# Performance work log

Measured on AMD Instinct MI355X. Metric: run time of the kernel, lower is better.

Reference implementation:

```python
import jax, jax.numpy as jnp
import numpy as np

B, S, H, D = 4, 1024, 20, 64
DM = H * D          # 1280 model dim
DF = 4 * DM         # 5120 ffn dim
EPS = 1e-5          # haiku LayerNorm default


def setup_inputs() -> dict:
    key = jax.random.key(0)
    ks = jax.random.split(key, 12)
    sc = 1.0 / np.sqrt(DM)
    return {
        "x": jax.random.normal(ks[0], (B, S, DM), jnp.float32),
        "ln1_scale": jnp.ones((DM,), jnp.float32),
        "ln1_offset": jnp.zeros((DM,), jnp.float32),
        "wq": jax.random.normal(ks[1], (DM, DM), jnp.float32) * sc,
        "bq": jnp.zeros((DM,), jnp.float32),
        "wk": jax.random.normal(ks[2], (DM, DM), jnp.float32) * sc,
        "bk": jnp.zeros((DM,), jnp.float32),
        "wv": jax.random.normal(ks[3], (DM, DM), jnp.float32) * sc,
        "bv": jnp.zeros((DM,), jnp.float32),
        "wo": jax.random.normal(ks[4], (DM, DM), jnp.float32) * sc,
        "bo": jnp.zeros((DM,), jnp.float32),
        "ln2_scale": jnp.ones((DM,), jnp.float32),
        "ln2_offset": jnp.zeros((DM,), jnp.float32),
        "fc1_w": jax.random.normal(ks[5], (DM, DF), jnp.float32) * sc,
        "fc1_b": jnp.zeros((DF,), jnp.float32),
        "fc2_w": jax.random.normal(ks[6], (DF, DM), jnp.float32) * (1.0 / np.sqrt(DF)),
        "fc2_b": jnp.zeros((DM,), jnp.float32),
    }


def _layer_norm(x, scale, offset):
    m = jnp.mean(x, axis=-1, keepdims=True)
    v = jnp.mean(jnp.square(x - m), axis=-1, keepdims=True)
    return (x - m) * jax.lax.rsqrt(v + EPS) * scale + offset


def reference(x, ln1_scale, ln1_offset, wq, bq, wk, bk, wv, bv, wo, bo,
              ln2_scale, ln2_offset, fc1_w, fc1_b, fc2_w, fc2_b):
    b, s, dm = x.shape
    # --- self-attention sub-block ---
    res = x
    h = _layer_norm(x, ln1_scale, ln1_offset)
    q = (h @ wq + bq).reshape(b, s, H, D)
    k = (h @ wk + bk).reshape(b, s, H, D)
    v = (h @ wv + bv).reshape(b, s, H, D)
    logits = jnp.einsum('bthd,bThd->bhtT', q, k) / jnp.sqrt(jnp.asarray(D, x.dtype))
    weights = jax.nn.softmax(logits, axis=-1)
    attn = jnp.einsum('bhtT,bThd->bthd', weights, v).reshape(b, s, dm)
    x = res + (attn @ wo + bo)
    # --- MLP sub-block ---
    res = x
    h = _layer_norm(x, ln2_scale, ln2_offset)
    h = jax.nn.gelu(h @ fc1_w + fc1_b, approximate=False)
    x = res + (h @ fc2_w + fc2_b)
    return x
```

## Files before the change

### kernel.cpp

```cpp
#include <hip/hip_runtime.h>
#include <hip/hip_bf16.h>

typedef __hip_bfloat16 bf16;
typedef __attribute__((ext_vector_type(8))) short short8;
typedef __attribute__((ext_vector_type(4))) float f32x4;
typedef __attribute__((ext_vector_type(4))) unsigned short u16x4;

#define DMODEL 1280
#define DFFN   5120
#define BATCH  4
#define SEQ    1024
#define NHEAD  20
#define HDIM   64
#define NROWS  (BATCH * SEQ)

#define GLDS(g, l) __builtin_amdgcn_global_load_lds(                            \
    (const __attribute__((address_space(1))) void*)(g),                         \
    (__attribute__((address_space(3))) void*)(l), 16, 0, 0)

static __device__ __forceinline__ short8 ds_read128(const bf16* p) {
    short8 r;
    asm volatile("ds_read_b128 %0, %1"
        : "=v"(r)
        : "v"((const __attribute__((address_space(3))) bf16*)p));
    return r;
}

__global__ __launch_bounds__(256) void prep_all(
    const float* __restrict__ wq, const float* __restrict__ wk,
    const float* __restrict__ wv, const float* __restrict__ wo,
    const float* __restrict__ fc1w, const float* __restrict__ fc2w,
    const float* __restrict__ bq, const float* __restrict__ bk,
    const float* __restrict__ bv,
    bf16* __restrict__ wqkvt, bf16* __restrict__ wot,
    bf16* __restrict__ fc1t, bf16* __restrict__ fc2t,
    float* __restrict__ bqkv)
{
    const int bid = blockIdx.x;
    if (bid == 19200) {
        for (int i = threadIdx.x; i < DMODEL; i += 256) {
            bqkv[i]              = bq[i];
            bqkv[DMODEL + i]     = bk[i];
            bqkv[2 * DMODEL + i] = bv[i];
        }
        return;
    }
    const float* in;
    bf16* out;
    int K, N, n0, k0;
    if (bid < 6400) {
        const int mat = bid / 1600, rem = bid % 1600;
        K = DMODEL; N = DMODEL;
        n0 = (rem % 40) * 32; k0 = (rem / 40) * 32;
        switch (mat) {
            case 0:  in = wq; out = wqkvt; break;
            case 1:  in = wk; out = wqkvt + (size_t)DMODEL * DMODEL; break;
            case 2:  in = wv; out = wqkvt + (size_t)2 * DMODEL * DMODEL; break;
            default: in = wo; out = wot; break;
        }
    } else if (bid < 12800) {
        const int rem = bid - 6400;
        K = DMODEL; N = DFFN; in = fc1w; out = fc1t;
        n0 = (rem % 160) * 32; k0 = (rem / 160) * 32;
    } else {
        const int rem = bid - 12800;
        K = DFFN; N = DMODEL; in = fc2w; out = fc2t;
        n0 = (rem % 40) * 32; k0 = (rem / 40) * 32;
    }
    __shared__ float tile[32][33];
    const int tx = threadIdx.x & 31;
    const int ty = threadIdx.x >> 5;
    for (int i = 0; i < 32; i += 8)
        tile[ty + i][tx] = in[(size_t)(k0 + ty + i) * N + (n0 + tx)];
    __syncthreads();
    for (int i = 0; i < 32; i += 8)
        out[(size_t)(n0 + ty + i) * K + (k0 + tx)] = __float2bfloat16(tile[tx][ty + i]);
}

__global__ __launch_bounds__(256) void ln_bf16(
    const float* __restrict__ x, const float* __restrict__ sc,
    const float* __restrict__ of, bf16* __restrict__ out)
{
    const int row = blockIdx.x;
    const float* xr = x + (size_t)row * DMODEL;
    float v[5];
    float s = 0.f, s2 = 0.f;
    for (int i = 0; i < 5; ++i) {
        v[i] = xr[threadIdx.x + i * 256];
        s += v[i];
        s2 += v[i] * v[i];
    }
    for (int off = 1; off < 64; off <<= 1) {
        s  += __shfl_xor(s, off);
        s2 += __shfl_xor(s2, off);
    }
    __shared__ float red[2][4];
    const int wid = threadIdx.x >> 6;
    if ((threadIdx.x & 63) == 0) { red[0][wid] = s; red[1][wid] = s2; }
    __syncthreads();
    s  = red[0][0] + red[0][1] + red[0][2] + red[0][3];
    s2 = red[1][0] + red[1][1] + red[1][2] + red[1][3];
    const float mean = s * (1.0f / DMODEL);
    const float var  = s2 * (1.0f / DMODEL) - mean * mean;
    const float rstd = rsqrtf(var + 1e-5f);
    for (int i = 0; i < 5; ++i) {
        const int c = threadIdx.x + i * 256;
        const float y = (v[i] - mean) * rstd * sc[c] + of[c];
        out[(size_t)row * DMODEL + c] = __float2bfloat16(y);
    }
}

__global__ __launch_bounds__(256) void reduce2_ln(
    const float* __restrict__ P, const float* __restrict__ bias,
    const float* __restrict__ res, float* __restrict__ x1,
    const float* __restrict__ sc, const float* __restrict__ of,
    bf16* __restrict__ h2)
{
    const int row = blockIdx.x;
    const size_t base = (size_t)row * DMODEL;
    const int MN = NROWS * DMODEL;
    float v[5];
    float s = 0.f, s2 = 0.f;
    for (int i = 0; i < 5; ++i) {
        const int c = threadIdx.x + i * 256;
        const float val = P[base + c] + P[MN + base + c] + bias[c] + res[base + c];
        v[i] = val;
        x1[base + c] = val;
        s += val;
        s2 += val * val;
    }
    for (int off = 1; off < 64; off <<= 1) {
        s  += __shfl_xor(s, off);
        s2 += __shfl_xor(s2, off);
    }
    __shared__ float red[2][4];
    const int wid = threadIdx.x >> 6;
    if ((threadIdx.x & 63) == 0) { red[0][wid] = s; red[1][wid] = s2; }
    __syncthreads();
    s  = red[0][0] + red[0][1] + red[0][2] + red[0][3];
    s2 = red[1][0] + red[1][1] + red[1][2] + red[1][3];
    const float mean = s * (1.0f / DMODEL);
    const float var  = s2 * (1.0f / DMODEL) - mean * mean;
    const float rstd = rsqrtf(var + 1e-5f);
    for (int i = 0; i < 5; ++i) {
        const int c = threadIdx.x + i * 256;
        const float y = (v[i] - mean) * rstd * sc[c] + of[c];
        h2[base + c] = __float2bfloat16(y);
    }
}

template <int EPI>
__global__ __launch_bounds__(512, 4) void gemm_big(
    const bf16* __restrict__ A, const bf16* __restrict__ Bt,
    const float* __restrict__ bias,
    bf16* __restrict__ Cb, float* __restrict__ Cf,
    int M, int N, int K, int klen)
{
    __shared__ bf16 As[2][128][32];
    __shared__ bf16 Bs[2][256][32];
    const int m0 = blockIdx.x * 128;
    const int n0 = blockIdx.y * 256;
    const int z  = blockIdx.z;
    const int kbeg = z * klen;

    const int tid  = threadIdx.x;
    const int lane = tid & 63;
    const int wid  = tid >> 6;
    const int wm   = (wid >> 2) * 64;
    const int wn   = (wid & 3) * 64;
    const int l15  = lane & 15;
    const int lq   = lane >> 4;

    f32x4 acc[4][4];
    #pragma unroll
    for (int i = 0; i < 4; ++i)
        #pragma unroll
        for (int j = 0; j < 4; ++j)
            acc[i][j] = (f32x4){0.f, 0.f, 0.f, 0.f};

    const int cph  = lane & 3;
    const int lrow = wid * 16 + (lane >> 2);
    const int cgl8 = (cph ^ ((lrow >> 1) & 3)) * 8;
    const int lcol = cph * 8;

    const bf16* aT = A  + (size_t)(m0 + lrow) * K + kbeg + cgl8;
    const bf16* bT = Bt + (size_t)(n0 + lrow) * K + kbeg + cgl8;
    const size_t rstep = (size_t)128 * K;

    GLDS(aT,         &As[0][lrow][lcol]);
    GLDS(bT,         &Bs[0][lrow][lcol]);
    GLDS(bT + rstep, &Bs[0][lrow + 128][lcol]);

    const int ca = (lq ^ ((l15 >> 1) & 3)) * 8;
    const int nIter = klen / 32;
    int buf = 0;
    for (int it = 0; it < nIter; ++it) {
        asm volatile("s_waitcnt vmcnt(0)" ::: "memory");
        __builtin_amdgcn_s_barrier();

        if (it + 1 < nIter) {
            const int k1 = (it + 1) * 32;
            GLDS(aT + k1,         &As[buf ^ 1][lrow][lcol]);
            GLDS(bT + k1,         &Bs[buf ^ 1][lrow][lcol]);
            GLDS(bT + k1 + rstep, &Bs[buf ^ 1][lrow + 128][lcol]);
        }

        short8 af[4], bfr[4];
        #pragma unroll
        for (int nt = 0; nt < 4; ++nt)
            bfr[nt] = ds_read128(&Bs[buf][wn + nt * 16 + l15][ca]);
        #pragma unroll
        for (int mt = 0; mt < 4; ++mt)
            af[mt] = ds_read128(&As[buf][wm + mt * 16 + l15][ca]);

        __builtin_amdgcn_s_setprio(1);
        asm volatile("s_waitcnt lgkmcnt(3)" ::: "memory");
        __builtin_amdgcn_sched_barrier(0);
        #pragma unroll
        for (int nt = 0; nt < 4; ++nt)
            acc[0][nt] = __builtin_amdgcn_mfma_f32_16x16x32_bf16(
                af[0], bfr[nt], acc[0][nt], 0, 0, 0);
        asm volatile("s_waitcnt lgkmcnt(2)" ::: "memory");
        __builtin_amdgcn_sched_barrier(0);
        #pragma unroll
        for (int nt = 0; nt < 4; ++nt)
            acc[1][nt] = __builtin_amdgcn_mfma_f32_16x16x32_bf16(
                af[1], bfr[nt], acc[1][nt], 0, 0, 0);
        asm volatile("s_waitcnt lgkmcnt(1)" ::: "memory");
        __builtin_amdgcn_sched_barrier(0);
        #pragma unroll
        for (int nt = 0; nt < 4; ++nt)
            acc[2][nt] = __builtin_amdgcn_mfma_f32_16x16x32_bf16(
                af[2], bfr[nt], acc[2][nt], 0, 0, 0);
        asm volatile("s_waitcnt lgkmcnt(0)" ::: "memory");
        __builtin_amdgcn_sched_barrier(0);
        #pragma unroll
        for (int nt = 0; nt < 4; ++nt)
            acc[3][nt] = __builtin_amdgcn_mfma_f32_16x16x32_bf16(
                af[3], bfr[nt], acc[3][nt], 0, 0, 0);
        __builtin_amdgcn_s_setprio(0);

        buf ^= 1;
    }

    float* Pf = Cf + (size_t)z * M * N;
    #pragma unroll
    for (int mt = 0; mt < 4; ++mt)
        #pragma unroll
        for (int nt = 0; nt < 4; ++nt)
            #pragma unroll
            for (int r = 0; r < 4; ++r) {
                const int row = m0 + wm + mt * 16 + lq * 4 + r;
                const int col = n0 + wn + nt * 16 + l15;
                if (EPI == 0) {
                    const float v = acc[mt][nt][r] + bias[col];
                    Cb[(size_t)row * N + col] = __float2bfloat16(v);
                } else if (EPI == 2) {
                    const float v = acc[mt][nt][r] + bias[col];
                    const float g = 0.5f * v * (1.0f + erff(v * 0.70710678118654752f));
                    Cb[(size_t)row * N + col] = __float2bfloat16(g);
                } else {
                    Pf[(size_t)row * N + col] = acc[mt][nt][r];
                }
            }
}

__global__ __launch_bounds__(256) void reduce2(
    const float* __restrict__ P, const float* __restrict__ bias,
    const float* __restrict__ res, float* __restrict__ out, int MN, int N)
{
    const int i = (blockIdx.x * 256 + threadIdx.x) * 4;
    if (i >= MN) return;
    const float4 p0 = *(const float4*)(P + i);
    const float4 p1 = *(const float4*)(P + MN + i);
    const float4 r  = *(const float4*)(res + i);
    const float4 b  = *(const float4*)(bias + (i % N));
    float4 o;
    o.x = p0.x + p1.x + r.x + b.x;
    o.y = p0.y + p1.y + r.y + b.y;
    o.z = p0.z + p1.z + r.z + b.z;
    o.w = p0.w + p1.w + r.w + b.w;
    *(float4*)(out + i) = o;
}

__global__ __launch_bounds__(256) void flash_attn(
    const bf16* __restrict__ qb, const bf16* __restrict__ kb,
    const bf16* __restrict__ vb, bf16* __restrict__ ob, int ldq)
{
    __shared__ bf16 Ks[2][64][64];
    __shared__ bf16 Vt[64][64];
    __shared__ bf16 Ps[4][16][64];

    const int bh = blockIdx.y;
    const int b  = bh / NHEAD;
    const int hh = bh % NHEAD;
    const int q0 = blockIdx.x * 64;
    const int tid  = threadIdx.x;
    const int lane = tid & 63;
    const int wid  = tid >> 6;
    const int l15  = lane & 15;
    const int lq   = lane >> 4;
    const int key  = l15 & 7;

    short8 qf[2];
    {
        const bf16* qp = qb + (size_t)(b * SEQ + q0 + wid * 16 + l15) * ldq
                         + hh * HDIM + lq * 8;
        for (int kk = 0; kk < 2; ++kk) {
            union { short8 v; bf16 h[8]; } u;
            u.v = *(const short8*)(qp + kk * 32);
            for (int j = 0; j < 8; ++j)
                u.h[j] = __float2bfloat16(__bfloat162float(u.h[j]) * 0.125f);
            qf[kk] = u.v;
        }
    }

    f32x4 o[4];
    for (int dt = 0; dt < 4; ++dt) o[dt] = (f32x4){0.f, 0.f, 0.f, 0.f};
    float lsum = 0.f;

    const int krow  = wid * 8 + (lane >> 3);
    const int kcgl8 = ((lane & 7) ^ (krow & 7)) * 8;
    const int kcph8 = (lane & 7) * 8;
    const int vd0  = (tid & 15) * 4;
    const int vkv0 = (tid >> 4) * 4;

    const bf16* kBase = kb + (size_t)(b * SEQ + krow) * ldq + hh * HDIM + kcgl8;
    const bf16* vBase = vb + (size_t)(b * SEQ + vkv0) * ldq + hh * HDIM + vd0;

    GLDS(kBase,                    &Ks[0][krow][kcph8]);
    GLDS(kBase + (size_t)32 * ldq, &Ks[0][krow + 32][kcph8]);
    u16x4 vr[4];
    for (int j = 0; j < 4; ++j)
        vr[j] = *(const u16x4*)(vBase + (size_t)j * ldq);

    const int nIter = SEQ / 64;
    for (int it = 0; it < nIter; ++it) {
        const int buf = it & 1;
        __syncthreads();
        for (int i = 0; i < 4; ++i) {
            u16x4 w = { vr[0][i], vr[1][i], vr[2][i], vr[3][i] };
            const int p = ((vkv0 >> 3) ^ ((vd0 + i) & 7)) * 8 + (vkv0 & 7);
            *(u16x4*)(&Vt[vd0 + i][p]) = w;
        }
        __syncthreads();

        if (it + 1 < nIter) {
            const size_t off = (size_t)(it + 1) * 64 * ldq;
            GLDS(kBase + off,                    &Ks[buf ^ 1][krow][kcph8]);
            GLDS(kBase + off + (size_t)32 * ldq, &Ks[buf ^ 1][krow + 32][kcph8]);
            for (int j = 0; j < 4; ++j)
                vr[j] = *(const u16x4*)(vBase + off + (size_t)j * ldq);
        }

        for (int mt = 0; mt < 4; ++mt) {
            const bf16* kp = &Ks[buf][mt * 16 + l15][0];
            const short8 kf0 = *(const short8*)(kp + ((0 + lq) ^ key) * 8);
            const short8 kf1 = *(const short8*)(kp + ((4 + lq) ^ key) * 8);
            f32x4 a = (f32x4){0.f, 0.f, 0.f, 0.f};
            a = __builtin_amdgcn_mfma_f32_16x16x32_bf16(kf0, qf[0], a, 0, 0, 0);
            a = __builtin_amdgcn_mfma_f32_16x16x32_bf16(kf1, qf[1], a, 0, 0, 0);
            union { u16x4 v; bf16 h[4]; } pk;
            for (int r = 0; r < 4; ++r) {
                const float p = __expf(a[r]);
                lsum += p;
                pk.h[r] = __float2bfloat16(p);
            }
            const int pc = ((mt * 2 + (lq >> 1)) ^ key) * 8 + (lq & 1) * 4;
            *(u16x4*)(&Ps[wid][l15][pc]) = pk.v;
        }

        for (int kk = 0; kk < 2; ++kk) {
            const short8 pf = *(const short8*)(
                &Ps[wid][l15][((lq + 4 * kk) ^ key) * 8]);
            for (int dt = 0; dt < 4; ++dt) {
                const short8 vf = *(const short8*)(
                    &Vt[dt * 16 + l15][((lq + 4 * kk) ^ key) * 8]);
                o[dt] = __builtin_amdgcn_mfma_f32_16x16x32_bf16(
                    vf, pf, o[dt], 0, 0, 0);
            }
        }
    }

    lsum += __shfl_xor(lsum, 16);
    lsum += __shfl_xor(lsum, 32);
    const float inv_l = 1.0f / lsum;

    const size_t qrow = (size_t)(b * SEQ + q0 + wid * 16 + l15);
    for (int dt = 0; dt < 4; ++dt) {
        union { u16x4 v; bf16 h[4]; } w;
        for (int r = 0; r < 4; ++r)
            w.h[r] = __float2bfloat16(o[dt][r] * inv_l);
        *(u16x4*)(ob + qrow * DMODEL + hh * HDIM + dt * 16 + lq * 4) = w.v;
    }
}

extern "C" void kernel_launch(void* const* d_in, const int* in_sizes, int n_in,
                              void* d_out, int out_size, void* d_ws, size_t ws_size,
                              hipStream_t stream)
{
    (void)in_sizes; (void)n_in; (void)out_size; (void)ws_size;
    const float* x    = (const float*)d_in[0];
    const float* ln1s = (const float*)d_in[1];
    const float* ln1o = (const float*)d_in[2];
    const float* wq   = (const float*)d_in[3];
    const float* bq   = (const float*)d_in[4];
    const float* wk   = (const float*)d_in[5];
    const float* bk   = (const float*)d_in[6];
    const float* wv   = (const float*)d_in[7];
    const float* bv   = (const float*)d_in[8];
    const float* wo   = (const float*)d_in[9];
    const float* bo   = (const float*)d_in[10];
    const float* ln2s = (const float*)d_in[11];
    const float* ln2o = (const float*)d_in[12];
    const float* fc1w = (const float*)d_in[13];
    const float* fc1b = (const float*)d_in[14];
    const float* fc2w = (const float*)d_in[15];
    const float* fc2b = (const float*)d_in[16];
    float* out = (float*)d_out;

    char* wp = (char*)d_ws;
    auto alloc = [&](size_t n) { char* p = wp; wp += (n + 255) & ~(size_t)255; return p; };
    bf16*  wqkvt = (bf16*)alloc((size_t)3 * DMODEL * DMODEL * 2);
    bf16*  wot   = (bf16*)alloc((size_t)DMODEL * DMODEL * 2);
    bf16*  fc1t  = (bf16*)alloc((size_t)DFFN * DMODEL * 2);
    bf16*  fc2t  = (bf16*)alloc((size_t)DMODEL * DFFN * 2);
    float* bqkv  = (float*)alloc((size_t)3 * DMODEL * 4);
    char*  regA  = alloc((size_t)NROWS * DMODEL * 2
                       + (size_t)NROWS * 3 * DMODEL * 2
                       + (size_t)NROWS * DMODEL * 2);
    bf16*  h     = (bf16*)regA;
    bf16*  qkv   = (bf16*)(regA + (size_t)NROWS * DMODEL * 2);
    bf16*  attn  = (bf16*)(regA + (size_t)NROWS * 4 * DMODEL * 2);
    float* part  = (float*)regA;
    bf16*  h2    = (bf16*)alloc((size_t)NROWS * DMODEL * 2);
    bf16*  g     = (bf16*)alloc((size_t)NROWS * DFFN * 2);
    float* x1    = out;

    prep_all<<<19201, 256, 0, stream>>>(
        wq, wk, wv, wo, fc1w, fc2w, bq, bk, bv,
        wqkvt, wot, fc1t, fc2t, bqkv);

    ln_bf16<<<NROWS, 256, 0, stream>>>(x, ln1s, ln1o, h);

    gemm_big<0><<<dim3(NROWS / 128, 3 * DMODEL / 256, 1), 512, 0, stream>>>(
        h, wqkvt, bqkv, qkv, nullptr, NROWS, 3 * DMODEL, DMODEL, DMODEL);

    flash_attn<<<dim3(SEQ / 64, BATCH * NHEAD), 256, 0, stream>>>(
        qkv, qkv + DMODEL, qkv + 2 * DMODEL, attn, 3 * DMODEL);

    gemm_big<3><<<dim3(NROWS / 128, DMODEL / 256, 2), 512, 0, stream>>>(
        attn, wot, nullptr, nullptr, part, NROWS, DMODEL, DMODEL, DMODEL / 2);
    reduce2_ln<<<NROWS, 256, 0, stream>>>(part, bo, x, x1, ln2s, ln2o, h2);

    gemm_big<2><<<dim3(NROWS / 128, DFFN / 256, 1), 512, 0, stream>>>(
        h2, fc1t, fc1b, g, nullptr, NROWS, DFFN, DMODEL, DMODEL);

    gemm_big<3><<<dim3(NROWS / 128, DMODEL / 256, 2), 512, 0, stream>>>(
        g, fc2t, nullptr, nullptr, part, NROWS, DMODEL, DFFN, DFFN / 2);
    reduce2<<<(NROWS * DMODEL / 4 + 255) / 256, 256, 0, stream>>>(
        part, fc2b, x1, out, NROWS * DMODEL, DMODEL);
}
```

Measured before the change: 466.4 us.

## Enlarge GEMM tiles to 256x256x64 with interleaved staging and LDS swizzle

Replaces the 128x256x32 GEMM with a 256x256 tile and K-step 64 kernel. It uses 128 KB of dynamic LDS, double-buffered stages prefetched two steps ahead, and a ping-pong schedule that interleaves A/B stage loads between MFMA quadrants under barriers. The aim is to cut global traffic per FLOP and LDS read overhead per MFMA. The cost is fewer blocks: the smaller GEMMs launch under one block per CU and occupancy drops, and register pressure rises from 32 accumulator tiles.

```diff
diff --git a/kernel.cpp b/kernel.cpp
--- a/kernel.cpp
+++ b/kernel.cpp
@@ -150,15 +150,18 @@
 }
 
 template <int EPI>
-__global__ __launch_bounds__(512, 4) void gemm_big(
+__global__ __launch_bounds__(512, 2) void gemm8p(
     const bf16* __restrict__ A, const bf16* __restrict__ Bt,
     const float* __restrict__ bias,
     bf16* __restrict__ Cb, float* __restrict__ Cf,
     int M, int N, int K, int klen)
 {
-    __shared__ bf16 As[2][128][32];
-    __shared__ bf16 Bs[2][256][32];
-    const int m0 = blockIdx.x * 128;
+    extern __shared__ char smem[];
+    constexpr int SLOT = 256 * 64;
+    bf16* As0 = (bf16*)smem;
+    bf16* Bs0 = As0 + 2 * SLOT;
+
+    const int m0 = blockIdx.x * 256;
     const int n0 = blockIdx.y * 256;
     const int z  = blockIdx.z;
     const int kbeg = z * klen;
@@ -166,86 +169,150 @@
     const int tid  = threadIdx.x;
     const int lane = tid & 63;
     const int wid  = tid >> 6;
-    const int wm   = (wid >> 2) * 64;
+    const int wm   = (wid >> 2) * 128;
     const int wn   = (wid & 3) * 64;
     const int l15  = lane & 15;
     const int lq   = lane >> 4;
 
-    f32x4 acc[4][4];
+    f32x4 acc[8][4];
     #pragma unroll
-    for (int i = 0; i < 4; ++i)
+    for (int i = 0; i < 8; ++i)
         #pragma unroll
         for (int j = 0; j < 4; ++j)
             acc[i][j] = (f32x4){0.f, 0.f, 0.f, 0.f};
 
-    const int cph  = lane & 3;
-    const int lrow = wid * 16 + (lane >> 2);
-    const int cgl8 = (cph ^ ((lrow >> 1) & 3)) * 8;
-    const int lcol = cph * 8;
-
-    const bf16* aT = A  + (size_t)(m0 + lrow) * K + kbeg + cgl8;
-    const bf16* bT = Bt + (size_t)(n0 + lrow) * K + kbeg + cgl8;
-    const size_t rstep = (size_t)128 * K;
-
-    GLDS(aT,         &As[0][lrow][lcol]);
-    GLDS(bT,         &Bs[0][lrow][lcol]);
-    GLDS(bT + rstep, &Bs[0][lrow + 128][lcol]);
-
-    const int ca = (lq ^ ((l15 >> 1) & 3)) * 8;
-    const int nIter = klen / 32;
-    int buf = 0;
-    for (int it = 0; it < nIter; ++it) {
-        asm volatile("s_waitcnt vmcnt(0)" ::: "memory");
+    const int srow = wid * 8 + (lane >> 3);
+    const int scl  = (lane & 7) ^ ((wid & 1) << 2) ^ (lane >> 4);
+    const bf16* aT = A  + (size_t)(m0 + srow) * K + kbeg + scl * 8;
+    const bf16* bT = Bt + (size_t)(n0 + srow) * K + kbeg + scl * 8;
+    const size_t rs64 = (size_t)64 * K;
+    const int dwave = (wid * 8) * 64;
+
+    auto STAGE_A = [&](int tt) {
+        const bf16* s = aT + (size_t)tt * 64;
+        bf16* d = As0 + (tt & 1) * SLOT + dwave;
+        GLDS(s,            d);
+        GLDS(s +     rs64, d +  64 * 64);
+        GLDS(s + 2 * rs64, d + 128 * 64);
+        GLDS(s + 3 * rs64, d + 192 * 64);
+    };
+    auto STAGE_B = [&](int tt) {
+        const bf16* s = bT + (size_t)tt * 64;
+        bf16* d = Bs0 + (tt & 1) * SLOT + dwave;
+        GLDS(s,            d);
+        GLDS(s +     rs64, d +  64 * 64);
+        GLDS(s + 2 * rs64, d + 128 * 64);
+        GLDS(s + 3 * rs64, d + 192 * 64);
+    };
+
+    const int rkey = (l15 >> 1) & 7;
+    const int pc0  = ((0 + lq) ^ rkey) * 8;
+    const int pc1  = ((4 + lq) ^ rkey) * 8;
+
+    STAGE_A(0); STAGE_B(0);
+    STAGE_A(1); STAGE_B(1);
+    asm volatile("s_waitcnt vmcnt(8)" ::: "memory");
+    __builtin_amdgcn_s_barrier();
+
+    const int T = klen / 64;
+    for (int t = 0; t < T; ++t) {
+        const int sl = t & 1;
+        bf16* Ac = As0 + sl * SLOT;
+        bf16* Bc = Bs0 + sl * SLOT;
+
+        short8 af[4][2], b0[2][2], b1[2][2];
+
+        #pragma unroll
+        for (int mt = 0; mt < 4; ++mt) {
+            const bf16* p = Ac + (size_t)(wm + mt * 16 + l15) * 64;
+            af[mt][0] = ds_read128(p + pc0);
+            af[mt][1] = ds_read128(p + pc1);
+        }
+        #pragma unroll
+        for (int nt = 0; nt < 2; ++nt) {
+            const bf16* p = Bc + (size_t)(wn + nt * 16 + l15) * 64;
+            b0[nt][0] = ds_read128(p + pc0);
+            b0[nt][1] = ds_read128(p + pc1);
+        }
+        #pragma unroll
+        for (int nt = 0; nt < 2; ++nt) {
+            const bf16* p = Bc + (size_t)(wn + 32 + nt * 16 + l15) * 64;
+            b1[nt][0] = ds_read128(p + pc0);
+            b1[nt][1] = ds_read128(p + pc1);
+        }
+        if (t >= 1 && t + 1 < T) STAGE_B(t + 1);
         __builtin_amdgcn_s_barrier();
-
-        if (it + 1 < nIter) {
-            const int k1 = (it + 1) * 32;
-            GLDS(aT + k1,         &As[buf ^ 1][lrow][lcol]);
-            GLDS(bT + k1,         &Bs[buf ^ 1][lrow][lcol]);
-            GLDS(bT + k1 + rstep, &Bs[buf ^ 1][lrow + 128][lcol]);
-        }
-
-        short8 af[4], bfr[4];
-        #pragma unroll
-        for (int nt = 0; nt < 4; ++nt)
-            bfr[nt] = ds_read128(&Bs[buf][wn + nt * 16 + l15][ca]);
-        #pragma unroll
-        for (int mt = 0; mt < 4; ++mt)
-            af[mt] = ds_read128(&As[buf][wm + mt * 16 + l15][ca]);
-
-        __builtin_amdgcn_s_setprio(1);
-        asm volatile("s_waitcnt lgkmcnt(3)" ::: "memory");
-        __builtin_amdgcn_sched_barrier(0);
-        #pragma unroll
-        for (int nt = 0; nt < 4; ++nt)
-            acc[0][nt] = __builtin_amdgcn_mfma_f32_16x16x32_bf16(
-                af[0], bfr[nt], acc[0][nt], 0, 0, 0);
-        asm volatile("s_waitcnt lgkmcnt(2)" ::: "memory");
-        __builtin_amdgcn_sched_barrier(0);
-        #pragma unroll
-        for (int nt = 0; nt < 4; ++nt)
-            acc[1][nt] = __builtin_amdgcn_mfma_f32_16x16x32_bf16(
-                af[1], bfr[nt], acc[1][nt], 0, 0, 0);
-        asm volatile("s_waitcnt lgkmcnt(1)" ::: "memory");
-        __builtin_amdgcn_sched_barrier(0);
-        #pragma unroll
-        for (int nt = 0; nt < 4; ++nt)
-            acc[2][nt] = __builtin_amdgcn_mfma_f32_16x16x32_bf16(
-                af[2], bfr[nt], acc[2][nt], 0, 0, 0);
         asm volatile("s_waitcnt lgkmcnt(0)" ::: "memory");
         __builtin_amdgcn_sched_barrier(0);
-        #pragma unroll
-        for (int nt = 0; nt < 4; ++nt)
-            acc[3][nt] = __builtin_amdgcn_mfma_f32_16x16x32_bf16(
-                af[3], bfr[nt], acc[3][nt], 0, 0, 0);
+        __builtin_amdgcn_s_setprio(1);
+        #pragma unroll
+        for (int mt = 0; mt < 4; ++mt)
+            #pragma unroll
+            for (int nt = 0; nt < 2; ++nt) {
+                acc[mt][nt] = __builtin_amdgcn_mfma_f32_16x16x32_bf16(
+                    af[mt][0], b0[nt][0], acc[mt][nt], 0, 0, 0);
+                acc[mt][nt] = __builtin_amdgcn_mfma_f32_16x16x32_bf16(
+                    af[mt][1], b0[nt][1], acc[mt][nt], 0, 0, 0);
+            }
         __builtin_amdgcn_s_setprio(0);
-
-        buf ^= 1;
+        __builtin_amdgcn_s_barrier();
+
+        __builtin_amdgcn_s_setprio(1);
+        #pragma unroll
+        for (int mt = 0; mt < 4; ++mt)
+            #pragma unroll
+            for (int nt = 0; nt < 2; ++nt) {
+                acc[mt][2 + nt] = __builtin_amdgcn_mfma_f32_16x16x32_bf16(
+                    af[mt][0], b1[nt][0], acc[mt][2 + nt], 0, 0, 0);
+                acc[mt][2 + nt] = __builtin_amdgcn_mfma_f32_16x16x32_bf16(
+                    af[mt][1], b1[nt][1], acc[mt][2 + nt], 0, 0, 0);
+            }
+        __builtin_amdgcn_s_setprio(0);
+
+        #pragma unroll
+        for (int mt = 0; mt < 4; ++mt) {
+            const bf16* p = Ac + (size_t)(wm + 64 + mt * 16 + l15) * 64;
+            af[mt][0] = ds_read128(p + pc0);
+            af[mt][1] = ds_read128(p + pc1);
+        }
+        __builtin_amdgcn_s_barrier();
+        asm volatile("s_waitcnt lgkmcnt(0)" ::: "memory");
+        __builtin_amdgcn_sched_barrier(0);
+        __builtin_amdgcn_s_setprio(1);
+        #pragma unroll
+        for (int mt = 0; mt < 4; ++mt)
+            #pragma unroll
+            for (int nt = 0; nt < 2; ++nt) {
+                acc[4 + mt][2 + nt] = __builtin_amdgcn_mfma_f32_16x16x32_bf16(
+                    af[mt][0], b1[nt][0], acc[4 + mt][2 + nt], 0, 0, 0);
+                acc[4 + mt][2 + nt] = __builtin_amdgcn_mfma_f32_16x16x32_bf16(
+                    af[mt][1], b1[nt][1], acc[4 + mt][2 + nt], 0, 0, 0);
+            }
+        __builtin_amdgcn_s_setprio(0);
+        __builtin_amdgcn_s_barrier();
+
+        if (t + 2 < T) STAGE_A(t + 2);
+        __builtin_amdgcn_s_setprio(1);
+        #pragma unroll
+        for (int mt = 0; mt < 4; ++mt)
+            #pragma unroll
+            for (int nt = 0; nt < 2; ++nt) {
+                acc[4 + mt][nt] = __builtin_amdgcn_mfma_f32_16x16x32_bf16(
+                    af[mt][0], b0[nt][0], acc[4 + mt][nt], 0, 0, 0);
+                acc[4 + mt][nt] = __builtin_amdgcn_mfma_f32_16x16x32_bf16(
+                    af[mt][1], b0[nt][1], acc[4 + mt][nt], 0, 0, 0);
+            }
+        __builtin_amdgcn_s_setprio(0);
+        if (t + 1 < T) {
+            if (t + 2 < T) asm volatile("s_waitcnt vmcnt(4)" ::: "memory");
+            else           asm volatile("s_waitcnt vmcnt(0)" ::: "memory");
+            __builtin_amdgcn_s_barrier();
+        }
     }
 
     float* Pf = Cf + (size_t)z * M * N;
     #pragma unroll
-    for (int mt = 0; mt < 4; ++mt)
+    for (int mt = 0; mt < 8; ++mt)
         #pragma unroll
         for (int nt = 0; nt < 4; ++nt)
             #pragma unroll
@@ -443,20 +510,20 @@
 
     ln_bf16<<<NROWS, 256, 0, stream>>>(x, ln1s, ln1o, h);
 
-    gemm_big<0><<<dim3(NROWS / 128, 3 * DMODEL / 256, 1), 512, 0, stream>>>(
+    gemm8p<0><<<dim3(NROWS / 256, 3 * DMODEL / 256, 1), 512, 131072, stream>>>(
         h, wqkvt, bqkv, qkv, nullptr, NROWS, 3 * DMODEL, DMODEL, DMODEL);
 
     flash_attn<<<dim3(SEQ / 64, BATCH * NHEAD), 256, 0, stream>>>(
         qkv, qkv + DMODEL, qkv + 2 * DMODEL, attn, 3 * DMODEL);
 
-    gemm_big<3><<<dim3(NROWS / 128, DMODEL / 256, 2), 512, 0, stream>>>(
+    gemm8p<3><<<dim3(NROWS / 256, DMODEL / 256, 2), 512, 131072, stream>>>(
         attn, wot, nullptr, nullptr, part, NROWS, DMODEL, DMODEL, DMODEL / 2);
     reduce2_ln<<<NROWS, 256, 0, stream>>>(part, bo, x, x1, ln2s, ln2o, h2);
 
-    gemm_big<2><<<dim3(NROWS / 128, DFFN / 256, 1), 512, 0, stream>>>(
+    gemm8p<2><<<dim3(NROWS / 256, DFFN / 256, 1), 512, 131072, stream>>>(
         h2, fc1t, fc1b, g, nullptr, NROWS, DFFN, DMODEL, DMODEL);
 
-    gemm_big<3><<<dim3(NROWS / 128, DMODEL / 256, 2), 512, 0, stream>>>(
+    gemm8p<3><<<dim3(NROWS / 256, DMODEL / 256, 2), 512, 131072, stream>>>(
         g, fc2t, nullptr, nullptr, part, NROWS, DMODEL, DFFN, DFFN / 2);
     reduce2<<<(NROWS * DMODEL / 4 + 255) / 256, 256, 0, stream>>>(
         part, fc2b, x1, out, NROWS * DMODEL, DMODEL);
```

Result: slower. 486.8 us (+4.4%).
